# Kernel optimization log

Measured on AMD Instinct MI355X. Metric: run time of the kernel, lower is better.

The kernel has to match this reference:

```python
import jax, jax.numpy as jnp
import numpy as np

H = 8          # attention heads
D = 16         # per-head dim (hidden // heads)
HID = 128      # hidden_channels
OUT = 8        # out_channels of final linear
L = 2          # num_layers
NP = 100000    # num paper nodes
NA = 100000    # num author nodes
E = 500000     # edges per edge type
NEG_SLOPE = 0.2


def setup_inputs() -> dict:
    key = jax.random.key(0)
    ks = jax.random.split(key, 20)
    def nrm(k, shape, s=0.05):
        return jax.random.normal(k, shape, dtype=jnp.float32) * s
    return {
        'x_paper': jax.random.normal(ks[0], (NP, HID), dtype=jnp.float32),
        'x_author': jax.random.normal(ks[1], (NA, HID), dtype=jnp.float32),
        'Wp_p': nrm(ks[2], (L, HID, HID)),
        'bp_p': jnp.zeros((L, HID), jnp.float32),
        'Wp_a': nrm(ks[3], (L, HID, HID)),
        'bp_a': jnp.zeros((L, HID), jnp.float32),
        'as_ap': nrm(ks[4], (L, H, D), 0.2),
        'ad_ap': nrm(ks[5], (L, H, D), 0.2),
        'as_pa': nrm(ks[6], (L, H, D), 0.2),
        'ad_pa': nrm(ks[7], (L, H, D), 0.2),
        'as_pp': nrm(ks[8], (L, H, D), 0.2),
        'ad_pp': nrm(ks[9], (L, H, D), 0.2),
        'Wk': nrm(ks[10], (L, HID, HID)),
        'bk': jnp.zeros((L, HID), jnp.float32),
        'q': nrm(ks[11], (L, HID), 0.2),
        'Wout': nrm(ks[12], (HID, OUT)),
        'bout': jnp.zeros((OUT,), jnp.float32),
        'ei_ap': jax.random.randint(ks[13], (2, E), 0, NP, dtype=jnp.int32),
        'ei_pa': jax.random.randint(ks[14], (2, E), 0, NP, dtype=jnp.int32),
        'ei_pp': jax.random.randint(ks[15], (2, E), 0, NP, dtype=jnp.int32),
    }


def _leaky_relu(x):
    return jnp.where(x >= 0, x, NEG_SLOPE * x)


def _seg_softmax(alpha, dst, n):
    # PyG-style segment softmax over incoming edges of each dst node
    amax = jax.ops.segment_max(alpha, dst, num_segments=n)
    a = jnp.exp(alpha - amax[dst])
    denom = jax.ops.segment_sum(a, dst, num_segments=n) + 1e-16
    return a / denom[dst]


def _edge_attn_agg(z_src, z_dst, ei, a_s, a_d, n_dst):
    # per-edge-type GAT-style attention + scatter aggregate (HANConv message/aggregate)
    src, dst = ei[0], ei[1]
    alpha_src = (z_src * a_s).sum(-1)   # [Ns, H]
    alpha_dst = (z_dst * a_d).sum(-1)   # [Nd, H]
    alpha = _leaky_relu(alpha_src[src] + alpha_dst[dst])  # [E, H]
    alpha = _seg_softmax(alpha, dst, n_dst)
    msg = z_src[src] * alpha[:, :, None]                   # [E, H, D]
    out = jax.ops.segment_sum(msg, dst, num_segments=n_dst)
    return jax.nn.relu(out.reshape(n_dst, H * D))


def _group(outs, q, Wk, bk):
    # HANConv semantic-level attention across metapaths
    stacked = jnp.stack(outs)                               # [K, N, F]
    score = (q * jnp.tanh(stacked @ Wk + bk).mean(1)).sum(-1)  # [K]
    attn = jax.nn.softmax(score)
    return (attn[:, None, None] * stacked).sum(0)           # [N, F]


def _han_conv(xp, xa, ei_ap, ei_pa, ei_pp, Wp_p, bp_p, Wp_a, bp_a,
              as_ap, ad_ap, as_pa, ad_pa, as_pp, ad_pp, Wk, bk, q):
    zp = (xp @ Wp_p + bp_p).reshape(-1, H, D)
    za = (xa @ Wp_a + bp_a).reshape(-1, H, D)
    n_p, n_a = zp.shape[0], za.shape[0]
    out_ap = _edge_attn_agg(za, zp, ei_ap, as_ap, ad_ap, n_p)  # author -> paper
    out_pa = _edge_attn_agg(zp, za, ei_pa, as_pa, ad_pa, n_a)  # paper -> author
    out_pp = _edge_attn_agg(zp, zp, ei_pp, as_pp, ad_pp, n_p)  # paper -> paper
    new_xp = _group([out_ap, out_pp], q, Wk, bk)
    new_xa = _group([out_pa], q, Wk, bk)
    return new_xp, new_xa


def _forward(x_paper, x_author, Wp_p, bp_p, Wp_a, bp_a, as_ap, ad_ap,
             as_pa, ad_pa, as_pp, ad_pp, Wk, bk, q, Wout, bout,
             ei_ap, ei_pa, ei_pp):
    xp, xa = x_paper, x_author
    for l in range(L):
        xp, xa = _han_conv(xp, xa, ei_ap, ei_pa, ei_pp,
                           Wp_p[l], bp_p[l], Wp_a[l], bp_a[l],
                           as_ap[l], ad_ap[l], as_pa[l], ad_pa[l],
                           as_pp[l], ad_pp[l], Wk[l], bk[l], q[l])
        if l < L - 1:
            xp = jax.nn.elu(xp)  # dropout identity in eval mode (p applied only in training)
            xa = jax.nn.elu(xa)
    tgt = jax.nn.elu(xp)
    return tgt @ Wout + bout  # [NP, OUT]


def reference(x_paper, x_author, Wp_p, bp_p, Wp_a, bp_a, as_ap, ad_ap,
              as_pa, ad_pa, as_pp, ad_pp, Wk, bk, q, Wout, bout,
              ei_ap, ei_pa, ei_pp):
    return _forward(x_paper, x_author, Wp_p, bp_p, Wp_a, bp_a, as_ap, ad_ap,
                    as_pa, ad_pa, as_pp, ad_pp, Wk, bk, q, Wout, bout,
                    ei_ap, ei_pa, ei_pp)
```

## Files before the change

### kernel.cpp

```cpp
#include <hip/hip_runtime.h>

#define NHID 128
#define NHEAD 8
#define NNODE 100000
#define NEDGE 500000
#define NEG 0.2f
#define SCORE_GRID 512
#define GEMM_GRID 512
#define AGG_BLOCKS 12500

typedef float4 f4;
typedef __attribute__((ext_vector_type(8))) short bfrag;
typedef __attribute__((ext_vector_type(4))) float facc;

__device__ inline float b2f(unsigned int u) {
    return __uint_as_float(u << 16);
}
__device__ inline unsigned short f2b(float f) {
    unsigned int u = __float_as_uint(f);
    unsigned int r = (u + 0x7FFFu + ((u >> 16) & 1u)) >> 16;
    return (unsigned short)r;
}
__device__ inline float fast_tanh(float x) {
    float e = __expf(2.f * x);
    return 1.f - 2.f / (e + 1.f);
}

__global__ __launch_bounds__(256) void cvt_wt6(
    const float* __restrict__ w0, const float* __restrict__ w1,
    const float* __restrict__ w2, const float* __restrict__ w3,
    const float* __restrict__ w4, const float* __restrict__ w5,
    ushort* __restrict__ o0, ushort* __restrict__ o1,
    ushort* __restrict__ o2, ushort* __restrict__ o3,
    ushort* __restrict__ o4, ushort* __restrict__ o5)
{
    int which = blockIdx.x >> 6;
    int i = (blockIdx.x & 63) * 256 + threadIdx.x;
    const float* W = (which == 0) ? w0 : (which == 1) ? w1 : (which == 2) ? w2
                   : (which == 3) ? w3 : (which == 4) ? w4 : w5;
    ushort* Wt = (which == 0) ? o0 : (which == 1) ? o1 : (which == 2) ? o2
               : (which == 3) ? o3 : (which == 4) ? o4 : o5;
    int fi = i >> 3, e = i & 7;
    int jk = fi >> 6, l = fi & 63;
    int j = jk >> 2, kk = jk & 3;
    int lr = l & 15, lg = l >> 4;
    Wt[i] = f2b(W[(kk * 32 + lg * 8 + e) * 128 + j * 16 + lr]);
}

struct WavSet {
    const float* W; const float* b;
    const float* v0; const float* v1; const float* v2; const float* v3;
    ushort* GT; float* bAv;
};

__global__ __launch_bounds__(256) void build_wav4(WavSet s0, WavSet s1, WavSet s2, WavSet s3)
{
    int which = blockIdx.x >> 4;
    const WavSet s = (which == 0) ? s0 : (which == 1) ? s1 : (which == 2) ? s2 : s3;
    int i = (blockIdx.x & 15) * 256 + threadIdx.x;
    int fi = i >> 3, e = i & 7;
    int jk = fi >> 6, l = fi & 63;
    int jt = jk >> 2, kk = jk & 3;
    int lr = l & 15, lg = l >> 4;
    int c = jt * 16 + lr;
    int m = kk * 32 + lg * 8 + e;
    int vec = c >> 3, h = c & 7;
    const float* vp = (vec == 0) ? s.v0 : (vec == 1) ? s.v1 : (vec == 2) ? s.v2 : s.v3;
    float sv = 0.f;
    if (vp) {
        #pragma unroll
        for (int dd = 0; dd < 16; ++dd)
            sv = fmaf(s.W[m * 128 + h * 16 + dd], vp[h * 16 + dd], sv);
    }
    s.GT[i] = f2b(sv);
    if (i < 32) {
        int cc = i, vv = cc >> 3, hh = cc & 7;
        const float* vq = (vv == 0) ? s.v0 : (vv == 1) ? s.v1 : (vv == 2) ? s.v2 : s.v3;
        float t = 0.f;
        if (vq) {
            #pragma unroll
            for (int dd = 0; dd < 16; ++dd)
                t = fmaf(s.b[hh * 16 + dd], vq[hh * 16 + dd], t);
        }
        s.bAv[cc] = t;
    }
}

struct PArgs {
    const void* A;
    const ushort* A2;
    const ushort* WtT;
    const ushort* GT;
    const float* bias;
    const float* bAv;
    ushort* C;
    float* ao0; float* ao1; float* ao2; float* ao3;
    int mode;
};

template<int M0, int M1>
__global__ __launch_bounds__(256) void gemm_persist(
    PArgs g0, PArgs g1, const float* __restrict__ attn, int nt, int N)
{
    __shared__ uint4 smem[2560];
    const int hg = gridDim.x >> 1;
    const int half = (blockIdx.x >= hg) ? 1 : 0;
    const PArgs ga = half ? g1 : g0;
    const int MODE = half ? M1 : M0;
    const int b0 = half ? blockIdx.x - hg : blockIdx.x;

    const int tid = threadIdx.x;
    const int l = tid & 63, w = tid >> 6;
    const int lr = l & 15, lg = l >> 4;

    {
        const uint4* ws = reinterpret_cast<const uint4*>(ga.WtT);
        const uint4* gs = reinterpret_cast<const uint4*>(ga.GT);
        #pragma unroll
        for (int i = 0; i < 8; ++i) smem[tid + i * 256] = ws[tid + i * 256];
        #pragma unroll
        for (int i = 0; i < 2; ++i) smem[2048 + tid + i * 256] = gs[tid + i * 256];
    }
    float a0 = 0.f, a1 = 0.f;
    if (MODE == 2) { a0 = attn[0]; a1 = attn[1]; }
    __syncthreads();
    const ushort* WtL = reinterpret_cast<const ushort*>(smem);
    const ushort* GL  = WtL + 16384;

    float bv[8];
    #pragma unroll
    for (int j = 0; j < 8; ++j) bv[j] = ga.bias[j * 16 + lr];
    float bA[2];
    #pragma unroll
    for (int jt = 0; jt < 2; ++jt) bA[jt] = ga.bAv[jt * 16 + lr];

    uint4 rawA[(M0 == 0 && M1 == 0) ? 8 : 16];

    auto load_raw = [&](int t) {
        const int rw0 = t * 128 + w * 32;
        #pragma unroll
        for (int i = 0; i < 2; ++i) {
            int r = rw0 + i * 16 + lr; r = (r < N) ? r : (N - 1);
            if (MODE == 1) {
                const float* ap = (const float*)ga.A + (size_t)r * 128 + lg * 8;
                #pragma unroll
                for (int kk = 0; kk < 4; ++kk) {
                    rawA[i * 8 + kk * 2]     = *reinterpret_cast<const uint4*>(ap + kk * 32);
                    rawA[i * 8 + kk * 2 + 1] = *reinterpret_cast<const uint4*>(ap + kk * 32 + 4);
                }
            } else {
                const ushort* ap = (const ushort*)ga.A + (size_t)r * 128 + lg * 8;
                #pragma unroll
                for (int kk = 0; kk < 4; ++kk)
                    rawA[i * 4 + kk] = *reinterpret_cast<const uint4*>(ap + kk * 32);
                if (MODE == 2) {
                    const ushort* ap2 = ga.A2 + (size_t)r * 128 + lg * 8;
                    #pragma unroll
                    for (int kk = 0; kk < 4; ++kk)
                        rawA[8 + i * 4 + kk] = *reinterpret_cast<const uint4*>(ap2 + kk * 32);
                }
            }
        }
    };

    if (b0 >= nt) return;
    load_raw(b0);

    for (int t = b0; t < nt; t += hg) {
        const int rw0 = t * 128 + w * 32;

        bfrag av_[2][4];
        #pragma unroll
        for (int i = 0; i < 2; ++i) {
            #pragma unroll
            for (int kk = 0; kk < 4; ++kk) {
                if (MODE == 0) {
                    av_[i][kk] = *reinterpret_cast<bfrag*>(&rawA[i * 4 + kk]);
                } else if (MODE == 1) {
                    uint4 u = rawA[i * 8 + kk * 2];
                    uint4 v = rawA[i * 8 + kk * 2 + 1];
                    bfrag fr;
                    fr[0] = (short)f2b(__uint_as_float(u.x));
                    fr[1] = (short)f2b(__uint_as_float(u.y));
                    fr[2] = (short)f2b(__uint_as_float(u.z));
                    fr[3] = (short)f2b(__uint_as_float(u.w));
                    fr[4] = (short)f2b(__uint_as_float(v.x));
                    fr[5] = (short)f2b(__uint_as_float(v.y));
                    fr[6] = (short)f2b(__uint_as_float(v.z));
                    fr[7] = (short)f2b(__uint_as_float(v.w));
                    av_[i][kk] = fr;
                } else {
                    uint4 ua = rawA[i * 4 + kk];
                    uint4 ub = rawA[8 + i * 4 + kk];
                    unsigned int aa[4] = {ua.x, ua.y, ua.z, ua.w};
                    unsigned int bb[4] = {ub.x, ub.y, ub.z, ub.w};
                    bfrag fr;
                    #pragma unroll
                    for (int q = 0; q < 4; ++q) {
                        float lo = a0 * b2f(aa[q] & 0xffffu) + a1 * b2f(bb[q] & 0xffffu);
                        float hi = a0 * b2f(aa[q] >> 16)     + a1 * b2f(bb[q] >> 16);
                        fr[q * 2]     = (short)f2b(lo);
                        fr[q * 2 + 1] = (short)f2b(hi);
                    }
                    av_[i][kk] = fr;
                }
            }
        }

        if (t + hg < nt) load_raw(t + hg);

        facc accC[2][8], accP[2][2];
        #pragma unroll
        for (int i = 0; i < 2; ++i) {
            #pragma unroll
            for (int j = 0; j < 8; ++j) accC[i][j] = (facc){0.f, 0.f, 0.f, 0.f};
            #pragma unroll
            for (int jt = 0; jt < 2; ++jt) accP[i][jt] = (facc){0.f, 0.f, 0.f, 0.f};
        }

        #pragma unroll
        for (int kk = 0; kk < 4; ++kk) {
            #pragma unroll
            for (int j = 0; j < 8; ++j) {
                bfrag bfr = *reinterpret_cast<const bfrag*>(WtL + ((j * 4 + kk) * 64 + l) * 8);
                #pragma unroll
                for (int i = 0; i < 2; ++i)
                    accC[i][j] = __builtin_amdgcn_mfma_f32_16x16x32_bf16(
                        av_[i][kk], bfr, accC[i][j], 0, 0, 0);
            }
            #pragma unroll
            for (int jt = 0; jt < 2; ++jt) {
                bfrag gfr = *reinterpret_cast<const bfrag*>(GL + ((jt * 4 + kk) * 64 + l) * 8);
                #pragma unroll
                for (int i = 0; i < 2; ++i)
                    accP[i][jt] = __builtin_amdgcn_mfma_f32_16x16x32_bf16(
                        av_[i][kk], gfr, accP[i][jt], 0, 0, 0);
            }
        }

        #pragma unroll
        for (int j = 0; j < 8; ++j) {
            #pragma unroll
            for (int i = 0; i < 2; ++i) {
                #pragma unroll
                for (int rr = 0; rr < 4; ++rr) {
                    int row = rw0 + i * 16 + lg * 4 + rr;
                    if (row < N)
                        ga.C[(size_t)row * 128 + j * 16 + lr] = f2b(accC[i][j][rr] + bv[j]);
                }
            }
        }

        #pragma unroll
        for (int jt = 0; jt < 2; ++jt) {
            int c = jt * 16 + lr;
            int vec = c >> 3, h = c & 7;
            float* ao = (vec == 0) ? ga.ao0 : (vec == 1) ? ga.ao1
                      : (vec == 2) ? ga.ao2 : ga.ao3;
            if (ao == nullptr) continue;
            #pragma unroll
            for (int i = 0; i < 2; ++i) {
                #pragma unroll
                for (int rr = 0; rr < 4; ++rr) {
                    int row = rw0 + i * 16 + lg * 4 + rr;
                    if (row < N) ao[row * 8 + h] = accP[i][jt][rr] + bA[jt];
                }
            }
        }
    }
}

__global__ __launch_bounds__(256) void score_persist(
    const ushort* __restrict__ A0, const ushort* __restrict__ A1,
    const ushort* __restrict__ WtT, const float* __restrict__ bias,
    float* __restrict__ part, int nt, int N)
{
    __shared__ uint4 smem[2048];
    __shared__ float sred[4][256];
    const int tid = threadIdx.x;
    const int l = tid & 63, w = tid >> 6;
    const int lr = l & 15, lg = l >> 4;

    {
        const uint4* ws = reinterpret_cast<const uint4*>(WtT);
        #pragma unroll
        for (int i = 0; i < 8; ++i) smem[tid + i * 256] = ws[tid + i * 256];
    }
    __syncthreads();
    const ushort* WtL = reinterpret_cast<const ushort*>(smem);

    float bv[8];
    #pragma unroll
    for (int j = 0; j < 8; ++j) bv[j] = bias[j * 16 + lr];

    float cs[2][8];
    #pragma unroll
    for (int h = 0; h < 2; ++h)
        #pragma unroll
        for (int j = 0; j < 8; ++j) cs[h][j] = 0.f;

    const int total = 2 * nt;
    for (int t = blockIdx.x; t < total; t += gridDim.x) {
        const int half = (t >= nt) ? 1 : 0;
        const ushort* A = half ? A1 : A0;
        const int bb = half ? t - nt : t;
        const int rw0 = bb * 128 + w * 32;

        bfrag av_[2][4];
        #pragma unroll
        for (int i = 0; i < 2; ++i) {
            int r = rw0 + i * 16 + lr; r = (r < N) ? r : (N - 1);
            const ushort* ap = A + (size_t)r * 128 + lg * 8;
            #pragma unroll
            for (int kk = 0; kk < 4; ++kk)
                av_[i][kk] = *reinterpret_cast<const bfrag*>(ap + kk * 32);
        }

        facc acc[2][8];
        #pragma unroll
        for (int i = 0; i < 2; ++i)
            #pragma unroll
            for (int j = 0; j < 8; ++j) acc[i][j] = (facc){0.f, 0.f, 0.f, 0.f};

        #pragma unroll
        for (int kk = 0; kk < 4; ++kk) {
            #pragma unroll
            for (int j = 0; j < 8; ++j) {
                bfrag bfr = *reinterpret_cast<const bfrag*>(WtL + ((j * 4 + kk) * 64 + l) * 8);
                #pragma unroll
                for (int i = 0; i < 2; ++i)
                    acc[i][j] = __builtin_amdgcn_mfma_f32_16x16x32_bf16(
                        av_[i][kk], bfr, acc[i][j], 0, 0, 0);
            }
        }

        #pragma unroll
        for (int j = 0; j < 8; ++j) {
            float s = 0.f;
            #pragma unroll
            for (int i = 0; i < 2; ++i) {
                #pragma unroll
                for (int r = 0; r < 4; ++r) {
                    int row = rw0 + i * 16 + lg * 4 + r;
                    if (row < N) s += fast_tanh(acc[i][j][r] + bv[j]);
                }
            }
            cs[half][j] += s;
        }
    }

    #pragma unroll
    for (int h = 0; h < 2; ++h)
        #pragma unroll
        for (int j = 0; j < 8; ++j) {
            float s = cs[h][j];
            s += __shfl_xor(s, 16, 64);
            s += __shfl_xor(s, 32, 64);
            if (lg == 0) sred[w][h * 128 + j * 16 + lr] = s;
        }
    __syncthreads();
    float tot = sred[0][tid] + sred[1][tid] + sred[2][tid] + sred[3][tid];
    part[(size_t)blockIdx.x * 256 + tid] = tot;
}

__global__ void attn_reduce(const float* __restrict__ part,
                            const float* __restrict__ qv,
                            float* __restrict__ attn, int nb)
{
    __shared__ float sm[256];
    int t = threadIdx.x;
    float s0 = 0.f, s1 = 0.f, s2 = 0.f, s3 = 0.f;
    for (int b = 0; b < nb; b += 4) {
        s0 += part[(size_t)b * 256 + t];
        s1 += part[(size_t)(b + 1) * 256 + t];
        s2 += part[(size_t)(b + 2) * 256 + t];
        s3 += part[(size_t)(b + 3) * 256 + t];
    }
    sm[t] = (s0 + s1 + s2 + s3) * qv[t & 127];
    __syncthreads();
    if (t == 0) {
        float a = 0.f, b = 0.f;
        for (int i = 0; i < 128; ++i) { a += sm[i]; b += sm[128 + i]; }
        a *= (1.0f / 100000.0f);
        b *= (1.0f / 100000.0f);
        float m = fmaxf(a, b);
        float ea = expf(a - m), eb = expf(b - m);
        float inv = 1.f / (ea + eb);
        attn[0] = ea * inv;
        attn[1] = eb * inv;
    }
}

#define EB ((NEDGE + 255) / 256)
#define SB ((NNODE + 1023) / 1024)

__global__ __launch_bounds__(256) void hist3(
    const int* __restrict__ e0, const int* __restrict__ e1, const int* __restrict__ e2,
    int* __restrict__ deg3)
{
    int ty = blockIdx.x / EB, bb = blockIdx.x % EB;
    const int* ei = (ty == 0) ? e0 : (ty == 1) ? e1 : e2;
    int e = bb * 256 + threadIdx.x;
    if (e < NEDGE) atomicAdd(deg3 + ty * NNODE + ei[NEDGE + e], 1);
}

__global__ __launch_bounds__(1024) void scan_block3(
    const int* __restrict__ deg3, int* __restrict__ offs3, int* __restrict__ bsum3)
{
    __shared__ int sd[1024];
    int ty = blockIdx.x / SB, bb = blockIdx.x % SB;
    const int* deg = deg3 + ty * NNODE;
    int* offs = offs3 + ty * (NNODE + 1);
    int t = threadIdx.x, i = bb * 1024 + t;
    int v = (i < NNODE) ? deg[i] : 0;
    sd[t] = v; __syncthreads();
    for (int o = 1; o < 1024; o <<= 1) {
        int x = (t >= o) ? sd[t - o] : 0;
        __syncthreads();
        sd[t] += x;
        __syncthreads();
    }
    if (i < NNODE) offs[i + 1] = sd[t];
    if (t == 1023) bsum3[ty * 128 + bb] = sd[t];
}

__global__ void scan_bsum3(const int* __restrict__ bsum3, int* __restrict__ boff3)
{
    int t = threadIdx.x;
    if (t < 3) {
        int run = 0;
        for (int b = 0; b < SB; ++b) { boff3[t * 128 + b] = run; run += bsum3[t * 128 + b]; }
    }
}

__global__ __launch_bounds__(1024) void scan_add3(
    int* __restrict__ offs3, const int* __restrict__ boff3, int* __restrict__ cur3)
{
    int ty = blockIdx.x / SB, bb = blockIdx.x % SB;
    int* offs = offs3 + ty * (NNODE + 1);
    int* cur = cur3 + ty * NNODE;
    int i = bb * 1024 + threadIdx.x;
    if (i == 0) { offs[0] = 0; cur[0] = 0; }
    if (i < NNODE) {
        int v = offs[i + 1] + boff3[ty * 128 + bb];
        offs[i + 1] = v;
        if (i + 1 < NNODE) cur[i + 1] = v;
    }
}

__global__ __launch_bounds__(256) void scatter3(
    const int* __restrict__ e0, const int* __restrict__ e1, const int* __restrict__ e2,
    int* __restrict__ cur3, int* __restrict__ cols3)
{
    int ty = blockIdx.x / EB, bb = blockIdx.x % EB;
    const int* ei = (ty == 0) ? e0 : (ty == 1) ? e1 : e2;
    int e = bb * 256 + threadIdx.x;
    if (e < NEDGE) {
        int d = ei[NEDGE + e];
        int pos = atomicAdd(cur3 + ty * NNODE + d, 1);
        cols3[ty * NEDGE + pos] = ei[e];
    }
}

struct AggJob {
    const int* offs; const int* cols;
    const float* asrc; const float* adst;
    const ushort* z; ushort* out;
};

__global__ __launch_bounds__(256) void agg_multi(AggJob j0, AggJob j1, AggJob j2)
{
    int jb = blockIdx.x / AGG_BLOCKS;
    const AggJob jj = (jb == 0) ? j0 : (jb == 1) ? j1 : j2;
    int bb = blockIdx.x - jb * AGG_BLOCKS;
    int w = threadIdx.x >> 6;
    int lane = threadIdx.x & 63;
    int halfid = lane >> 5;
    int sl = lane & 31;
    int d = bb * 8 + w * 2 + halfid;
    int h = sl >> 2;
    float ad = jj.adst[d * 8 + h];
    int e0 = jj.offs[d], e1 = jj.offs[d + 1];
    float acc0 = 0.f, acc1 = 0.f, acc2 = 0.f, acc3 = 0.f, psum = 0.f;
    const ushort* zbase = jj.z + sl * 4;
    for (int base = e0; base < e1; base += 4) {
        int idx[4];
        #pragma unroll
        for (int i = 0; i < 4; ++i) {
            int ee = base + i;
            idx[i] = jj.cols[(ee < e1) ? ee : (e1 - 1)];
        }
        float xs[4];
        #pragma unroll
        for (int i = 0; i < 4; ++i) xs[i] = jj.asrc[idx[i] * 8 + h];
        uint2 zv[4];
        #pragma unroll
        for (int i = 0; i < 4; ++i)
            zv[i] = *reinterpret_cast<const uint2*>(zbase + (size_t)idx[i] * 128);
        #pragma unroll
        for (int i = 0; i < 4; ++i) {
            float a = xs[i] + ad;
            a = fmaxf(a, NEG * a);
            float p = __expf(a);
            p = (base + i < e1) ? p : 0.f;
            acc0 = fmaf(p, b2f(zv[i].x & 0xffffu), acc0);
            acc1 = fmaf(p, b2f(zv[i].x >> 16),     acc1);
            acc2 = fmaf(p, b2f(zv[i].y & 0xffffu), acc2);
            acc3 = fmaf(p, b2f(zv[i].y >> 16),     acc3);
            psum += p;
        }
    }
    float inv = 1.f / (psum + 1e-16f);
    uint2 pk;
    pk.x = (unsigned int)f2b(fmaxf(acc0 * inv, 0.f))
         | ((unsigned int)f2b(fmaxf(acc1 * inv, 0.f)) << 16);
    pk.y = (unsigned int)f2b(fmaxf(acc2 * inv, 0.f))
         | ((unsigned int)f2b(fmaxf(acc3 * inv, 0.f)) << 16);
    *reinterpret_cast<uint2*>(jj.out + (size_t)d * 128 + sl * 4) = pk;
}

__global__ __launch_bounds__(256) void final_gemm_mix(
    const ushort* __restrict__ XA_, const ushort* __restrict__ XB_,
    const float* __restrict__ attn, const float* __restrict__ W,
    const float* __restrict__ bias, float* __restrict__ out, int N)
{
    __shared__ float Ws[128][8];
    __shared__ __align__(16) float Xs[32][129];
    int tid = threadIdx.x;
    float a0 = attn[0], a1 = attn[1];
    for (int i = tid; i < 1024; i += 256) Ws[i >> 3][i & 7] = W[i];
    int row0 = blockIdx.x * 32;
    for (int i = tid; i < 512; i += 256) {
        int r = i >> 4, q = i & 15;
        int gr = row0 + r;
        uint4 va = make_uint4(0, 0, 0, 0), vb = make_uint4(0, 0, 0, 0);
        if (gr < N) {
            va = reinterpret_cast<const uint4*>(XA_ + (size_t)gr * 128)[q];
            vb = reinterpret_cast<const uint4*>(XB_ + (size_t)gr * 128)[q];
        }
        int c = q * 8;
        unsigned int ua[4] = {va.x, va.y, va.z, va.w};
        unsigned int ub[4] = {vb.x, vb.y, vb.z, vb.w};
        #pragma unroll
        for (int qq = 0; qq < 4; ++qq) {
            Xs[r][c + qq * 2]     = a0 * b2f(ua[qq] & 0xffffu) + a1 * b2f(ub[qq] & 0xffffu);
            Xs[r][c + qq * 2 + 1] = a0 * b2f(ua[qq] >> 16)     + a1 * b2f(ub[qq] >> 16);
        }
    }
    __syncthreads();
    int r = tid >> 3, o = tid & 7;
    int gr = row0 + r;
    if (gr < N) {
        float s = bias[o];
        #pragma unroll
        for (int k = 0; k < 128; ++k) s = fmaf(Xs[r][k], Ws[k][o], s);
        out[(size_t)gr * 8 + o] = s;
    }
}

extern "C" void kernel_launch(void* const* d_in, const int* in_sizes, int n_in,
                              void* d_out, int out_size, void* d_ws, size_t ws_size,
                              hipStream_t stream) {
    const float* x_paper  = (const float*)d_in[0];
    const float* x_author = (const float*)d_in[1];
    const float* Wp_p = (const float*)d_in[2];
    const float* bp_p = (const float*)d_in[3];
    const float* Wp_a = (const float*)d_in[4];
    const float* bp_a = (const float*)d_in[5];
    const float* as_ap = (const float*)d_in[6];
    const float* ad_ap = (const float*)d_in[7];
    const float* as_pa = (const float*)d_in[8];
    const float* ad_pa = (const float*)d_in[9];
    const float* as_pp = (const float*)d_in[10];
    const float* ad_pp = (const float*)d_in[11];
    const float* Wk   = (const float*)d_in[12];
    const float* bk   = (const float*)d_in[13];
    const float* qv   = (const float*)d_in[14];
    const float* Wout = (const float*)d_in[15];
    const float* bout = (const float*)d_in[16];
    const int* ei_ap = (const int*)d_in[17];
    const int* ei_pa = (const int*)d_in[18];
    const int* ei_pp = (const int*)d_in[19];

    const size_t NB = (size_t)NNODE * 128;
    ushort* Z0 = (ushort*)d_ws;
    ushort* Z1 = Z0 + NB;
    ushort* Z2 = Z1 + NB;
    ushort* Z3 = Z2 + NB;
    ushort* P0 = Z3 + NB;
    ushort* P1 = P0 + NB;
    float* fp = (float*)(P1 + NB);
    float* ap_s = fp; fp += NNODE * 8;
    float* ap_d = fp; fp += NNODE * 8;
    float* pa_s = fp; fp += NNODE * 8;
    float* pa_d = fp; fp += NNODE * 8;
    float* pp_s = fp; fp += NNODE * 8;
    float* pp_d = fp; fp += NNODE * 8;
    float* part = fp; fp += (size_t)SCORE_GRID * 256;
    float* attn = fp; fp += 16;
    float* bAv_p0 = fp; fp += 32;
    float* bAv_a0 = fp; fp += 32;
    float* bAv_p1 = fp; fp += 32;
    float* bAv_a1 = fp; fp += 32;
    ushort* up = (ushort*)fp;
    ushort* WtP0 = up; up += 16384;
    ushort* WtA0 = up; up += 16384;
    ushort* WtP1 = up; up += 16384;
    ushort* WtA1 = up; up += 16384;
    ushort* WtK0 = up; up += 16384;
    ushort* WtK1 = up; up += 16384;
    ushort* G_p0 = up; up += 4096;
    ushort* G_a0 = up; up += 4096;
    ushort* G_p1 = up; up += 4096;
    ushort* G_a1 = up; up += 4096;
    int* ip = (int*)(((size_t)up + 15) & ~(size_t)15);
    int* cols3 = ip; ip += 3 * NEDGE;
    int* offs3 = ip; ip += 3 * (NNODE + 1);
    int* deg3  = ip; ip += 3 * NNODE;
    int* cur3  = ip; ip += 3 * NNODE;
    int* bsum3 = ip; ip += 3 * 128;
    int* boff3 = ip; ip += 3 * 128;

    const int* cols_ap = cols3;
    const int* cols_pa = cols3 + NEDGE;
    const int* cols_pp = cols3 + 2 * NEDGE;
    const int* offs_ap = offs3;
    const int* offs_pa = offs3 + (NNODE + 1);
    const int* offs_pp = offs3 + 2 * (NNODE + 1);

    const dim3 blk(256);
    const int nt128 = (NNODE + 127) / 128;
    const int wo = 128 * 128, bo = 128, ao = 128;

    cvt_wt6<<<384, blk, 0, stream>>>(Wp_p, Wp_a, Wp_p + wo, Wp_a + wo, Wk, Wk + wo,
                                     WtP0, WtA0, WtP1, WtA1, WtK0, WtK1);
    {
        WavSet s0{Wp_p, bp_p, ad_ap, as_pa, as_pp, ad_pp, G_p0, bAv_p0};
        WavSet s1{Wp_a, bp_a, as_ap, ad_pa, nullptr, nullptr, G_a0, bAv_a0};
        WavSet s2{Wp_p + wo, bp_p + bo, ad_ap + ao, as_pp + ao, ad_pp + ao, nullptr, G_p1, bAv_p1};
        WavSet s3{Wp_a + wo, bp_a + bo, as_ap + ao, nullptr, nullptr, nullptr, G_a1, bAv_a1};
        build_wav4<<<64, blk, 0, stream>>>(s0, s1, s2, s3);
    }

    hipMemsetAsync(deg3, 0, 3 * NNODE * 4, stream);
    hist3<<<3 * EB, blk, 0, stream>>>(ei_ap, ei_pa, ei_pp, deg3);
    scan_block3<<<3 * SB, 1024, 0, stream>>>(deg3, offs3, bsum3);
    scan_bsum3<<<1, 64, 0, stream>>>(bsum3, boff3);
    scan_add3<<<3 * SB, 1024, 0, stream>>>(offs3, boff3, cur3);
    scatter3<<<3 * EB, blk, 0, stream>>>(ei_ap, ei_pa, ei_pp, cur3, cols3);

    {
        PArgs gp{x_paper,  nullptr, WtP0, G_p0, bp_p, bAv_p0, Z0, ap_d, pa_s, pp_s, pp_d, 1};
        PArgs ga{x_author, nullptr, WtA0, G_a0, bp_a, bAv_a0, Z1, ap_s, pa_d, nullptr, nullptr, 1};
        gemm_persist<1, 1><<<GEMM_GRID, blk, 0, stream>>>(gp, ga, attn, nt128, NNODE);
    }

    {
        AggJob a0{offs_ap, cols_ap, ap_s, ap_d, Z1, Z2};
        AggJob a1{offs_pa, cols_pa, pa_s, pa_d, Z0, Z3};
        AggJob a2{offs_pp, cols_pp, pp_s, pp_d, Z0, P0};
        agg_multi<<<3 * AGG_BLOCKS, blk, 0, stream>>>(a0, a1, a2);
    }

    score_persist<<<SCORE_GRID, blk, 0, stream>>>(Z2, P0, WtK0, bk, part, nt128, NNODE);
    attn_reduce<<<1, 256, 0, stream>>>(part, qv, attn, SCORE_GRID);

    {
        PArgs gp{Z2, P0, WtP1, G_p1, bp_p + bo, bAv_p1, Z0, ap_d, pp_s, pp_d, nullptr, 2};
        PArgs ga{Z3, nullptr, WtA1, G_a1, bp_a + bo, bAv_a1, Z1, ap_s, nullptr, nullptr, nullptr, 0};
        gemm_persist<2, 0><<<GEMM_GRID, blk, 0, stream>>>(gp, ga, attn, nt128, NNODE);
    }

    {
        AggJob a0{offs_ap, cols_ap, ap_s, ap_d, Z1, Z2};
        AggJob a1{offs_pp, cols_pp, pp_s, pp_d, Z0, P1};
        agg_multi<<<2 * AGG_BLOCKS, blk, 0, stream>>>(a0, a1, a1);
    }

    score_persist<<<SCORE_GRID, blk, 0, stream>>>(Z2, P1, WtK1, bk + bo, part, nt128, NNODE);
    attn_reduce<<<1, 256, 0, stream>>>(part, qv + bo, attn, SCORE_GRID);

    final_gemm_mix<<<(NNODE + 31) / 32, blk, 0, stream>>>(Z2, P1, attn, Wout, bout, (float*)d_out, NNODE);
}
```

Measured before the change: 579.1 us.

## Fuse weight prep with degree histogram and overlap CSR scatter with first GEMM

Merges the weight-conversion, attention-weight build and degree-histogram kernels into one launch. The edge scatter that fills the CSR columns now runs as extra blocks inside the first projection GEMM launch, so the two can overlap. This removes three launches and lets the independent scatter work share the GPU with the GEMM. The cost is a larger, more branchy grid, and the GEMM's half-split index is now fixed to GEMM_GRID instead of gridDim.

```diff
diff --git a/kernel.cpp b/kernel.cpp
--- a/kernel.cpp
+++ b/kernel.cpp
@@ -8,6 +8,8 @@
 #define SCORE_GRID 512
 #define GEMM_GRID 512
 #define AGG_BLOCKS 12500
+#define EB ((NEDGE + 255) / 256)
+#define SB ((NNODE + 1023) / 1024)
 
 typedef float4 f4;
 typedef __attribute__((ext_vector_type(8))) short bfrag;
@@ -26,63 +28,73 @@
     return 1.f - 2.f / (e + 1.f);
 }
 
-__global__ __launch_bounds__(256) void cvt_wt6(
+struct WavSet {
+    const float* W; const float* b;
+    const float* v0; const float* v1; const float* v2; const float* v3;
+    ushort* GT; float* bAv;
+};
+
+__global__ __launch_bounds__(256) void prep_fused(
     const float* __restrict__ w0, const float* __restrict__ w1,
     const float* __restrict__ w2, const float* __restrict__ w3,
     const float* __restrict__ w4, const float* __restrict__ w5,
     ushort* __restrict__ o0, ushort* __restrict__ o1,
     ushort* __restrict__ o2, ushort* __restrict__ o3,
-    ushort* __restrict__ o4, ushort* __restrict__ o5)
-{
-    int which = blockIdx.x >> 6;
-    int i = (blockIdx.x & 63) * 256 + threadIdx.x;
-    const float* W = (which == 0) ? w0 : (which == 1) ? w1 : (which == 2) ? w2
-                   : (which == 3) ? w3 : (which == 4) ? w4 : w5;
-    ushort* Wt = (which == 0) ? o0 : (which == 1) ? o1 : (which == 2) ? o2
-               : (which == 3) ? o3 : (which == 4) ? o4 : o5;
-    int fi = i >> 3, e = i & 7;
-    int jk = fi >> 6, l = fi & 63;
-    int j = jk >> 2, kk = jk & 3;
-    int lr = l & 15, lg = l >> 4;
-    Wt[i] = f2b(W[(kk * 32 + lg * 8 + e) * 128 + j * 16 + lr]);
-}
-
-struct WavSet {
-    const float* W; const float* b;
-    const float* v0; const float* v1; const float* v2; const float* v3;
-    ushort* GT; float* bAv;
-};
-
-__global__ __launch_bounds__(256) void build_wav4(WavSet s0, WavSet s1, WavSet s2, WavSet s3)
-{
-    int which = blockIdx.x >> 4;
-    const WavSet s = (which == 0) ? s0 : (which == 1) ? s1 : (which == 2) ? s2 : s3;
-    int i = (blockIdx.x & 15) * 256 + threadIdx.x;
-    int fi = i >> 3, e = i & 7;
-    int jk = fi >> 6, l = fi & 63;
-    int jt = jk >> 2, kk = jk & 3;
-    int lr = l & 15, lg = l >> 4;
-    int c = jt * 16 + lr;
-    int m = kk * 32 + lg * 8 + e;
-    int vec = c >> 3, h = c & 7;
-    const float* vp = (vec == 0) ? s.v0 : (vec == 1) ? s.v1 : (vec == 2) ? s.v2 : s.v3;
-    float sv = 0.f;
-    if (vp) {
-        #pragma unroll
-        for (int dd = 0; dd < 16; ++dd)
-            sv = fmaf(s.W[m * 128 + h * 16 + dd], vp[h * 16 + dd], sv);
-    }
-    s.GT[i] = f2b(sv);
-    if (i < 32) {
-        int cc = i, vv = cc >> 3, hh = cc & 7;
-        const float* vq = (vv == 0) ? s.v0 : (vv == 1) ? s.v1 : (vv == 2) ? s.v2 : s.v3;
-        float t = 0.f;
-        if (vq) {
+    ushort* __restrict__ o4, ushort* __restrict__ o5,
+    WavSet s0, WavSet s1, WavSet s2, WavSet s3,
+    const int* __restrict__ e0, const int* __restrict__ e1,
+    const int* __restrict__ e2, int* __restrict__ deg3)
+{
+    const int b = blockIdx.x;
+    if (b < 384) {
+        int which = b >> 6;
+        int i = (b & 63) * 256 + threadIdx.x;
+        const float* W = (which == 0) ? w0 : (which == 1) ? w1 : (which == 2) ? w2
+                       : (which == 3) ? w3 : (which == 4) ? w4 : w5;
+        ushort* Wt = (which == 0) ? o0 : (which == 1) ? o1 : (which == 2) ? o2
+                   : (which == 3) ? o3 : (which == 4) ? o4 : o5;
+        int fi = i >> 3, e = i & 7;
+        int jk = fi >> 6, l = fi & 63;
+        int j = jk >> 2, kk = jk & 3;
+        int lr = l & 15, lg = l >> 4;
+        Wt[i] = f2b(W[(kk * 32 + lg * 8 + e) * 128 + j * 16 + lr]);
+    } else if (b < 448) {
+        int bb = b - 384;
+        int which = bb >> 4;
+        const WavSet s = (which == 0) ? s0 : (which == 1) ? s1 : (which == 2) ? s2 : s3;
+        int i = (bb & 15) * 256 + threadIdx.x;
+        int fi = i >> 3, e = i & 7;
+        int jk = fi >> 6, l = fi & 63;
+        int jt = jk >> 2, kk = jk & 3;
+        int lr = l & 15, lg = l >> 4;
+        int c = jt * 16 + lr;
+        int m = kk * 32 + lg * 8 + e;
+        int vec = c >> 3, h = c & 7;
+        const float* vp = (vec == 0) ? s.v0 : (vec == 1) ? s.v1 : (vec == 2) ? s.v2 : s.v3;
+        float sv = 0.f;
+        if (vp) {
             #pragma unroll
             for (int dd = 0; dd < 16; ++dd)
-                t = fmaf(s.b[hh * 16 + dd], vq[hh * 16 + dd], t);
-        }
-        s.bAv[cc] = t;
+                sv = fmaf(s.W[m * 128 + h * 16 + dd], vp[h * 16 + dd], sv);
+        }
+        s.GT[i] = f2b(sv);
+        if (i < 32) {
+            int cc = i, vv = cc >> 3, hh = cc & 7;
+            const float* vq = (vv == 0) ? s.v0 : (vv == 1) ? s.v1 : (vv == 2) ? s.v2 : s.v3;
+            float t = 0.f;
+            if (vq) {
+                #pragma unroll
+                for (int dd = 0; dd < 16; ++dd)
+                    t = fmaf(s.b[hh * 16 + dd], vq[hh * 16 + dd], t);
+            }
+            s.bAv[cc] = t;
+        }
+    } else {
+        int bb2 = b - 448;
+        int ty = bb2 / EB, bb = bb2 % EB;
+        const int* ei = (ty == 0) ? e0 : (ty == 1) ? e1 : e2;
+        int e = bb * 256 + threadIdx.x;
+        if (e < NEDGE) atomicAdd(deg3 + ty * NNODE + ei[NEDGE + e], 1);
     }
 }
 
@@ -98,12 +110,27 @@
     int mode;
 };
 
-template<int M0, int M1>
+template<int M0, int M1, int SCAT>
 __global__ __launch_bounds__(256) void gemm_persist(
-    PArgs g0, PArgs g1, const float* __restrict__ attn, int nt, int N)
-{
+    PArgs g0, PArgs g1, const float* __restrict__ attn, int nt, int N,
+    const int* __restrict__ e0, const int* __restrict__ e1,
+    const int* __restrict__ e2, int* __restrict__ cur3, int* __restrict__ cols3)
+{
+    if (SCAT && blockIdx.x >= GEMM_GRID) {
+        int bb2 = blockIdx.x - GEMM_GRID;
+        int ty = bb2 / EB, bb = bb2 % EB;
+        const int* ei = (ty == 0) ? e0 : (ty == 1) ? e1 : e2;
+        int e = bb * 256 + threadIdx.x;
+        if (e < NEDGE) {
+            int d = ei[NEDGE + e];
+            int pos = atomicAdd(cur3 + ty * NNODE + d, 1);
+            cols3[ty * NEDGE + pos] = ei[e];
+        }
+        return;
+    }
+
     __shared__ uint4 smem[2560];
-    const int hg = gridDim.x >> 1;
+    const int hg = GEMM_GRID >> 1;
     const int half = (blockIdx.x >= hg) ? 1 : 0;
     const PArgs ga = half ? g1 : g0;
     const int MODE = half ? M1 : M0;
@@ -391,19 +418,6 @@
     }
 }
 
-#define EB ((NEDGE + 255) / 256)
-#define SB ((NNODE + 1023) / 1024)
-
-__global__ __launch_bounds__(256) void hist3(
-    const int* __restrict__ e0, const int* __restrict__ e1, const int* __restrict__ e2,
-    int* __restrict__ deg3)
-{
-    int ty = blockIdx.x / EB, bb = blockIdx.x % EB;
-    const int* ei = (ty == 0) ? e0 : (ty == 1) ? e1 : e2;
-    int e = bb * 256 + threadIdx.x;
-    if (e < NEDGE) atomicAdd(deg3 + ty * NNODE + ei[NEDGE + e], 1);
-}
-
 __global__ __launch_bounds__(1024) void scan_block3(
     const int* __restrict__ deg3, int* __restrict__ offs3, int* __restrict__ bsum3)
 {
@@ -445,20 +459,6 @@
         int v = offs[i + 1] + boff3[ty * 128 + bb];
         offs[i + 1] = v;
         if (i + 1 < NNODE) cur[i + 1] = v;
-    }
-}
-
-__global__ __launch_bounds__(256) void scatter3(
-    const int* __restrict__ e0, const int* __restrict__ e1, const int* __restrict__ e2,
-    int* __restrict__ cur3, int* __restrict__ cols3)
-{
-    int ty = blockIdx.x / EB, bb = blockIdx.x % EB;
-    const int* ei = (ty == 0) ? e0 : (ty == 1) ? e1 : e2;
-    int e = bb * 256 + threadIdx.x;
-    if (e < NEDGE) {
-        int d = ei[NEDGE + e];
-        int pos = atomicAdd(cur3 + ty * NNODE + d, 1);
-        cols3[ty * NEDGE + pos] = ei[e];
     }
 }
 
@@ -632,27 +632,26 @@
     const int nt128 = (NNODE + 127) / 128;
     const int wo = 128 * 128, bo = 128, ao = 128;
 
-    cvt_wt6<<<384, blk, 0, stream>>>(Wp_p, Wp_a, Wp_p + wo, Wp_a + wo, Wk, Wk + wo,
-                                     WtP0, WtA0, WtP1, WtA1, WtK0, WtK1);
+    hipMemsetAsync(deg3, 0, 3 * NNODE * 4, stream);
     {
         WavSet s0{Wp_p, bp_p, ad_ap, as_pa, as_pp, ad_pp, G_p0, bAv_p0};
         WavSet s1{Wp_a, bp_a, as_ap, ad_pa, nullptr, nullptr, G_a0, bAv_a0};
         WavSet s2{Wp_p + wo, bp_p + bo, ad_ap + ao, as_pp + ao, ad_pp + ao, nullptr, G_p1, bAv_p1};
         WavSet s3{Wp_a + wo, bp_a + bo, as_ap + ao, nullptr, nullptr, nullptr, G_a1, bAv_a1};
-        build_wav4<<<64, blk, 0, stream>>>(s0, s1, s2, s3);
-    }
-
-    hipMemsetAsync(deg3, 0, 3 * NNODE * 4, stream);
-    hist3<<<3 * EB, blk, 0, stream>>>(ei_ap, ei_pa, ei_pp, deg3);
+        prep_fused<<<448 + 3 * EB, blk, 0, stream>>>(
+            Wp_p, Wp_a, Wp_p + wo, Wp_a + wo, Wk, Wk + wo,
+            WtP0, WtA0, WtP1, WtA1, WtK0, WtK1,
+            s0, s1, s2, s3, ei_ap, ei_pa, ei_pp, deg3);
+    }
     scan_block3<<<3 * SB, 1024, 0, stream>>>(deg3, offs3, bsum3);
     scan_bsum3<<<1, 64, 0, stream>>>(bsum3, boff3);
     scan_add3<<<3 * SB, 1024, 0, stream>>>(offs3, boff3, cur3);
-    scatter3<<<3 * EB, blk, 0, stream>>>(ei_ap, ei_pa, ei_pp, cur3, cols3);
 
     {
         PArgs gp{x_paper,  nullptr, WtP0, G_p0, bp_p, bAv_p0, Z0, ap_d, pa_s, pp_s, pp_d, 1};
         PArgs ga{x_author, nullptr, WtA0, G_a0, bp_a, bAv_a0, Z1, ap_s, pa_d, nullptr, nullptr, 1};
-        gemm_persist<1, 1><<<GEMM_GRID, blk, 0, stream>>>(gp, ga, attn, nt128, NNODE);
+        gemm_persist<1, 1, 1><<<GEMM_GRID + 3 * EB, blk, 0, stream>>>(
+            gp, ga, attn, nt128, NNODE, ei_ap, ei_pa, ei_pp, cur3, cols3);
     }
 
     {
@@ -668,7 +667,8 @@
     {
         PArgs gp{Z2, P0, WtP1, G_p1, bp_p + bo, bAv_p1, Z0, ap_d, pp_s, pp_d, nullptr, 2};
         PArgs ga{Z3, nullptr, WtA1, G_a1, bp_a + bo, bAv_a1, Z1, ap_s, nullptr, nullptr, nullptr, 0};
-        gemm_persist<2, 0><<<GEMM_GRID, blk, 0, stream>>>(gp, ga, attn, nt128, NNODE);
+        gemm_persist<2, 0, 0><<<GEMM_GRID, blk, 0, stream>>>(
+            gp, ga, attn, nt128, NNODE, nullptr, nullptr, nullptr, nullptr, nullptr);
     }
 
     {
```

New measurement: 532.4 us. 1.09x faster.
